# Performance work log

Measured on AMD Instinct MI355X. Metric: run time of the kernel, lower is better.

The kernel has to match this reference:

```python
import jax, jax.numpy as jnp
import numpy as np
from jax import lax

C = 512          # in_channels = n_feats of EDSR upsampler
HEADS = 8
NUM_SA = 8
NB = 8           # EDSR resblocks (assumed; source of make_edsr_baseline not provided)
NCLS = 6
SCALE = 2        # EDSR upsampling factor
IN_SCOPE = [(-51.2, 51.2, 3.2), (-51.2, 51.2, 3.2)]
OUT_SCOPE = [(-50.0, 50.0, 2.0), (-50.0, 50.0, 2.0)]


def setup_inputs() -> dict:
    key = jax.random.key(0)
    ks = jax.random.split(key, 16)
    n = lambda k, s: jax.random.normal(k, s, jnp.float32)
    s_lin = C ** -0.5
    s_c3 = (C * 9) ** -0.5
    d = {}
    d['x'] = n(ks[0], (1, C, 32, 32))
    # attention params (weights stored as (in, out) for direct matmul)
    d['qkv_w'] = n(ks[1], (NUM_SA, C, 3 * C)) * s_lin
    d['proj_w'] = n(ks[2], (NUM_SA, C, C)) * s_lin
    d['proj_b'] = jnp.zeros((NUM_SA, C), jnp.float32)
    # EDSR baseline params (OIHW conv kernels)
    d['head_w'] = n(ks[3], (C, C, 3, 3)) * s_c3
    d['head_b'] = jnp.zeros((C,), jnp.float32)
    d['body_w'] = n(ks[4], (NB, 2, C, C, 3, 3)) * s_c3
    d['body_b'] = jnp.zeros((NB, 2, C), jnp.float32)
    d['btail_w'] = n(ks[5], (C, C, 3, 3)) * s_c3
    d['btail_b'] = jnp.zeros((C,), jnp.float32)
    d['up_w'] = n(ks[6], (SCALE * SCALE * C, C, 3, 3)) * s_c3
    d['up_b'] = jnp.zeros((SCALE * SCALE * C,), jnp.float32)
    d['tail_w'] = n(ks[7], (C, C, 3, 3)) * s_c3
    d['tail_b'] = jnp.zeros((C,), jnp.float32)
    # classifier_hr: conv3(no bias)-BN-ReLU x2 + conv1
    d['c1_w'] = n(ks[8], (C, C, 3, 3)) * s_c3
    d['bn1_g'] = jnp.ones((C,), jnp.float32)
    d['bn1_b'] = jnp.zeros((C,), jnp.float32)
    d['bn1_m'] = jnp.zeros((C,), jnp.float32)
    d['bn1_v'] = jnp.ones((C,), jnp.float32)
    d['c2_w'] = n(ks[9], (C, C, 3, 3)) * s_c3
    d['bn2_g'] = jnp.ones((C,), jnp.float32)
    d['bn2_b'] = jnp.zeros((C,), jnp.float32)
    d['bn2_m'] = jnp.zeros((C,), jnp.float32)
    d['bn2_v'] = jnp.ones((C,), jnp.float32)
    d['c3_w'] = n(ks[10], (NCLS, C, 1, 1)) * s_lin
    d['c3_b'] = jnp.zeros((NCLS,), jnp.float32)
    return d


def _conv(x, w, b=None, pad=1):
    y = lax.conv_general_dilated(x, w, (1, 1), [(pad, pad), (pad, pad)],
                                 dimension_numbers=('NCHW', 'OIHW', 'NCHW'))
    return y if b is None else y + b[None, :, None, None]


def _bn(x, g, b, m, v):
    scale = (g / jnp.sqrt(v + 1e-5))[None, :, None, None]
    return (x - m[None, :, None, None]) * scale + b[None, :, None, None]


def _pixel_shuffle(x, r):
    B, Cr2, H, W = x.shape
    c = Cr2 // (r * r)
    return x.reshape(B, c, r, r, H, W).transpose(0, 1, 4, 2, 5, 3).reshape(B, c, H * r, W * r)


def _grid_idx(size, inscope, outscope):
    # nearest-neighbor grid_sample indices, align_corners=False, zeros padding
    imin, imax, _ = inscope
    omin, omax, ostep = outscope
    vv = jnp.arange(omin + ostep / 2, omax, ostep, dtype=jnp.float32)
    g = (vv - imin) / (imax - imin) * 2 - 1              # normalized coord in [-1,1]
    f = ((g + 1) * size - 1) / 2                          # unnormalize (align_corners=False)
    ii = jnp.round(f).astype(jnp.int32)
    valid = (ii >= 0) & (ii < size)
    return jnp.clip(ii, 0, size - 1), valid


def reference(x, qkv_w, proj_w, proj_b, head_w, head_b, body_w, body_b, btail_w, btail_b,
              up_w, up_b, tail_w, tail_b, c1_w, bn1_g, bn1_b, bn1_m, bn1_v,
              c2_w, bn2_g, bn2_b, bn2_m, bn2_v, c3_w, c3_b):
    B, Cc, H, W = x.shape
    hd = Cc // HEADS
    scale = Cc ** -0.5  # NOTE: source scales by in_channels**-0.5, not head_dim
    # --- num_sa manual self-attention blocks over H*W tokens ---
    for i in range(NUM_SA):
        t = x.reshape(B, Cc, H * W).transpose(0, 2, 1)            # (B, N, C)
        qkv = (t @ qkv_w[i]).reshape(B, H * W, 3, HEADS, hd).transpose(2, 0, 3, 1, 4)
        q, k, v = qkv[0], qkv[1], qkv[2]                          # (B, h, N, d)
        attn = jax.nn.softmax(jnp.einsum('bhnd,bhmd->bhnm', q, k) * scale, axis=-1)
        res = jnp.einsum('bhnm,bhmd->bhnd', attn, v).transpose(0, 2, 1, 3).reshape(B, H * W, Cc)
        res = (res @ proj_w[i] + proj_b[i]).reshape(B, H, W, Cc).transpose(0, 3, 1, 2)
        x = x + res
    # --- BEVGridTransform: nearest grid_sample ---
    iy, my = _grid_idx(H, IN_SCOPE[0], OUT_SCOPE[0])
    ix, mx = _grid_idx(W, IN_SCOPE[1], OUT_SCOPE[1])
    xs = x[:, :, iy[:, None], ix[None, :]] * (my[:, None] & mx[None, :]).astype(x.dtype)
    xs = lax.stop_gradient(xs)  # upsampler(x.detach())
    # --- EDSR baseline upsampler ---
    h = _conv(xs, head_w, head_b)
    r = h
    for i in range(NB):
        t = jax.nn.relu(_conv(r, body_w[i, 0], body_b[i, 0]))
        r = r + _conv(t, body_w[i, 1], body_b[i, 1])
    r = _conv(r, btail_w, btail_b) + h
    u = _pixel_shuffle(_conv(r, up_w, up_b), SCALE)
    y = _conv(u, tail_w, tail_b)
    # --- classifier_hr (BN in eval mode) ---
    y = jax.nn.relu(_bn(_conv(y, c1_w), bn1_g, bn1_b, bn1_m, bn1_v))
    y = jax.nn.relu(_bn(_conv(y, c2_w), bn2_g, bn2_b, bn2_m, bn2_v))
    y = _conv(y, c3_w, c3_b, pad=0)
    return jax.nn.sigmoid(y)  # eval path: (1, 6, 100, 100)
```

## Files before the change

kernel.cpp:

```cpp
#include <hip/hip_runtime.h>
#include <math.h>

#define DIV_UP(a,b) (((a)+(b)-1)/(b))

typedef __bf16 bf16x8 __attribute__((ext_vector_type(8)));
typedef float floatx4 __attribute__((ext_vector_type(4)));
typedef unsigned short u16;

__device__ __forceinline__ u16 f2bf(float f) {
    unsigned u = __builtin_bit_cast(unsigned, f);
    u = (u + 0x7fffu + ((u >> 16) & 1u)) >> 16;
    return (u16)u;
}
__device__ __forceinline__ float bf2f(u16 h) {
    unsigned u = ((unsigned)h) << 16;
    return __builtin_bit_cast(float, u);
}

__device__ __forceinline__ void gll16(const void* g, void* l) {
    __builtin_amdgcn_global_load_lds(
        (const __attribute__((address_space(1))) void*)g,
        (__attribute__((address_space(3))) void*)l, 16, 0, 0);
}

template<int BM, int BN, int GWM, int GWN>
__global__ __launch_bounds__(256) void gemm3_nt(
    const u16* __restrict__ Ah, const u16* __restrict__ Al,
    int lda, long long a_bs,
    const u16* __restrict__ Bh, const u16* __restrict__ Bl,
    int ldb, long long b_bs,
    float* C, u16* Ch, u16* Cl, int ldc, long long c_bs,
    const float* resid, int M, int N, int K, float alpha,
    const float* __restrict__ bias_m, const float* __restrict__ scale_m,
    const float* __restrict__ bias_n, int relu)
{
    constexpr int WTM = BM / GWM, WTN = BN / GWN;
    constexpr int TM = WTM / 16, TN = WTN / 16;
    __shared__ u16 Ash[BM * 32];
    __shared__ u16 Asl[BM * 32];
    __shared__ u16 Bsh[BN * 32];
    __shared__ u16 Bsl[BN * 32];
    const int tid = threadIdx.x;
    const int lane = tid & 63;
    const int w = tid >> 6;
    const int wm = (w % GWM) * WTM, wn = (w / GWM) * WTN;
    const int m0 = blockIdx.y * BM, n0 = blockIdx.x * BN;
    const int z = blockIdx.z;
    const u16* Ahb = Ah + (long long)z * a_bs;
    const u16* Alb = Al + (long long)z * a_bs;
    const u16* Bhb = Bh + (long long)z * b_bs;
    const u16* Blb = Bl + (long long)z * b_bs;
    const int quad = lane >> 4;

    floatx4 acc[TM][TN];
    #pragma unroll
    for (int i = 0; i < TM; ++i)
        #pragma unroll
        for (int j = 0; j < TN; ++j)
            #pragma unroll
            for (int r = 0; r < 4; ++r) acc[i][j][r] = 0.f;

    for (int kt = 0; kt < K; kt += 32) {
        #pragma unroll
        for (int p = 0; p < BM / 64; ++p) {
            int idx = p * 256 + tid;
            int row = idx >> 2;
            int olog = (idx & 3) ^ ((row >> 1) & 3);
            int gr = m0 + row; if (gr > M - 1) gr = M - 1;
            long long go = (long long)gr * lda + kt + olog * 8;
            gll16(Ahb + go, &Ash[idx * 8]);
            gll16(Alb + go, &Asl[idx * 8]);
        }
        #pragma unroll
        for (int p = 0; p < BN / 64; ++p) {
            int idx = p * 256 + tid;
            int row = idx >> 2;
            int olog = (idx & 3) ^ ((row >> 1) & 3);
            int gr = n0 + row; if (gr > N - 1) gr = N - 1;
            long long go = (long long)gr * ldb + kt + olog * 8;
            gll16(Bhb + go, &Bsh[idx * 8]);
            gll16(Blb + go, &Bsl[idx * 8]);
        }
        __syncthreads();

        bf16x8 afh[TM], afl[TM], bfh[TN], bfl[TN];
        #pragma unroll
        for (int i = 0; i < TM; ++i) {
            int row = wm + i * 16 + (lane & 15);
            int oph = quad ^ ((row >> 1) & 3);
            afh[i] = *(const bf16x8*)&Ash[row * 32 + oph * 8];
            afl[i] = *(const bf16x8*)&Asl[row * 32 + oph * 8];
        }
        #pragma unroll
        for (int j = 0; j < TN; ++j) {
            int row = wn + j * 16 + (lane & 15);
            int oph = quad ^ ((row >> 1) & 3);
            bfh[j] = *(const bf16x8*)&Bsh[row * 32 + oph * 8];
            bfl[j] = *(const bf16x8*)&Bsl[row * 32 + oph * 8];
        }
        #pragma unroll
        for (int i = 0; i < TM; ++i)
            #pragma unroll
            for (int j = 0; j < TN; ++j) {
                acc[i][j] = __builtin_amdgcn_mfma_f32_16x16x32_bf16(afh[i], bfl[j], acc[i][j], 0, 0, 0);
                acc[i][j] = __builtin_amdgcn_mfma_f32_16x16x32_bf16(afl[i], bfh[j], acc[i][j], 0, 0, 0);
                acc[i][j] = __builtin_amdgcn_mfma_f32_16x16x32_bf16(afh[i], bfh[j], acc[i][j], 0, 0, 0);
            }
        __syncthreads();
    }

    #pragma unroll
    for (int i = 0; i < TM; ++i) {
        int mbase = m0 + wm + i * 16 + quad * 4;
        #pragma unroll
        for (int j = 0; j < TN; ++j) {
            int n = n0 + wn + j * 16 + (lane & 15);
            if (n >= N) continue;
            float bn_ = bias_n ? bias_n[n] : 0.f;
            #pragma unroll
            for (int r = 0; r < 4; ++r) {
                int m = mbase + r;
                if (m >= M) continue;
                float t = acc[i][j][r] * alpha;
                if (scale_m) t *= scale_m[m];
                if (bias_m)  t += bias_m[m];
                t += bn_;
                long long idx = (long long)z * c_bs + (long long)m * ldc + n;
                if (resid) t += resid[idx];
                if (relu) t = fmaxf(t, 0.f);
                if (C)  C[idx] = t;
                if (Ch) {
                    u16 h = f2bf(t);
                    Ch[idx] = h;
                    Cl[idx] = f2bf(t - bf2f(h));
                }
            }
        }
    }
}

template<int BM, int BN, int GWM, int GWN>
__global__ __launch_bounds__(256) void conv_gemm(
    const u16* __restrict__ Ih, const u16* __restrict__ Il,
    const u16* __restrict__ Wh, const u16* __restrict__ Wl,
    int Wd, int pW, int M, int N, int kper,
    float* __restrict__ Cp,
    float* __restrict__ C, u16* __restrict__ Ph, u16* __restrict__ Pl,
    const float* __restrict__ resid, const float* __restrict__ bias_n,
    const float* __restrict__ scale_n, int relu)
{
    constexpr int WTM = BM / GWM, WTN = BN / GWN;
    constexpr int TM = WTM / 16, TN = WTN / 16;
    __shared__ u16 Ash[BM * 32];
    __shared__ u16 Asl[BM * 32];
    __shared__ u16 Bsh[BN * 32];
    __shared__ u16 Bsl[BN * 32];
    const int tid = threadIdx.x;
    const int lane = tid & 63;
    const int w = tid >> 6;
    const int wm = (w % GWM) * WTM, wn = (w / GWM) * WTN;
    const int m0 = blockIdx.y * BM, n0 = blockIdx.x * BN;
    const int quad = lane >> 4;

    long aoff[BM / 64];
    #pragma unroll
    for (int p = 0; p < BM / 64; ++p) {
        int idx = p * 256 + tid;
        int row = idx >> 2;
        int olog = (idx & 3) ^ ((row >> 1) & 3);
        int gr = m0 + row; if (gr > M - 1) gr = M - 1;
        int hh = gr / Wd, ww = gr - hh * Wd;
        aoff[p] = ((long)(hh + 1) * pW + (ww + 1)) * 512 + olog * 8;
    }
    long boff[BN / 64];
    #pragma unroll
    for (int p = 0; p < BN / 64; ++p) {
        int idx = p * 256 + tid;
        int row = idx >> 2;
        int olog = (idx & 3) ^ ((row >> 1) & 3);
        int gn = n0 + row; if (gn > N - 1) gn = N - 1;
        boff[p] = (long)gn * 4608 + olog * 8;
    }

    floatx4 acc[TM][TN];
    #pragma unroll
    for (int i = 0; i < TM; ++i)
        #pragma unroll
        for (int j = 0; j < TN; ++j)
            #pragma unroll
            for (int r = 0; r < 4; ++r) acc[i][j][r] = 0.f;

    const int k0 = blockIdx.z * kper, k1 = k0 + kper;
    for (int kt = k0; kt < k1; kt += 32) {
        int r = kt >> 9;
        int rd = r / 3;
        long roff = ((long)(rd - 1) * pW + (r - 3 * rd - 1)) * 512 + (kt & 511);
        #pragma unroll
        for (int p = 0; p < BM / 64; ++p) {
            long go = aoff[p] + roff;
            gll16(Ih + go, &Ash[(p * 256 + tid) * 8]);
            gll16(Il + go, &Asl[(p * 256 + tid) * 8]);
        }
        #pragma unroll
        for (int p = 0; p < BN / 64; ++p) {
            long go = boff[p] + kt;
            gll16(Wh + go, &Bsh[(p * 256 + tid) * 8]);
            gll16(Wl + go, &Bsl[(p * 256 + tid) * 8]);
        }
        __syncthreads();

        bf16x8 afh[TM], afl[TM], bfh[TN], bfl[TN];
        #pragma unroll
        for (int i = 0; i < TM; ++i) {
            int row = wm + i * 16 + (lane & 15);
            int oph = quad ^ ((row >> 1) & 3);
            afh[i] = *(const bf16x8*)&Ash[row * 32 + oph * 8];
            afl[i] = *(const bf16x8*)&Asl[row * 32 + oph * 8];
        }
        #pragma unroll
        for (int j = 0; j < TN; ++j) {
            int row = wn + j * 16 + (lane & 15);
            int oph = quad ^ ((row >> 1) & 3);
            bfh[j] = *(const bf16x8*)&Bsh[row * 32 + oph * 8];
            bfl[j] = *(const bf16x8*)&Bsl[row * 32 + oph * 8];
        }
        #pragma unroll
        for (int i = 0; i < TM; ++i)
            #pragma unroll
            for (int j = 0; j < TN; ++j) {
                acc[i][j] = __builtin_amdgcn_mfma_f32_16x16x32_bf16(afh[i], bfl[j], acc[i][j], 0, 0, 0);
                acc[i][j] = __builtin_amdgcn_mfma_f32_16x16x32_bf16(afl[i], bfh[j], acc[i][j], 0, 0, 0);
                acc[i][j] = __builtin_amdgcn_mfma_f32_16x16x32_bf16(afh[i], bfh[j], acc[i][j], 0, 0, 0);
            }
        __syncthreads();
    }

    const long zoff = (long)blockIdx.z * M * N;
    #pragma unroll
    for (int i = 0; i < TM; ++i) {
        int mbase = m0 + wm + i * 16 + quad * 4;
        #pragma unroll
        for (int j = 0; j < TN; ++j) {
            int n = n0 + wn + j * 16 + (lane & 15);
            if (n >= N) continue;
            float bn_ = bias_n ? bias_n[n] : 0.f;
            float sn_ = scale_n ? scale_n[n] : 1.f;
            #pragma unroll
            for (int rr = 0; rr < 4; ++rr) {
                int m = mbase + rr;
                if (m >= M) continue;
                long li = (long)m * N + n;
                if (Cp) { Cp[zoff + li] = acc[i][j][rr]; continue; }
                float t = acc[i][j][rr] * sn_ + bn_;
                if (resid) t += resid[li];
                if (relu) t = fmaxf(t, 0.f);
                if (C) C[li] = t;
                if (Ph) {
                    int hh = m / Wd, ww = m - hh * Wd;
                    long po = ((long)(hh + 1) * pW + ww + 1) * N + n;
                    u16 h2 = f2bf(t);
                    Ph[po] = h2;
                    Pl[po] = f2bf(t - bf2f(h2));
                }
            }
        }
    }
}

__global__ __launch_bounds__(256) void reduce_ep(
    const float* __restrict__ Cp, int KS, int M, int N, int Wd, int pW,
    float* __restrict__ C, u16* __restrict__ Ph, u16* __restrict__ Pl,
    const float* __restrict__ resid, const float* __restrict__ bias_n,
    const float* __restrict__ scale_n, int relu)
{
    long i4 = (long)blockIdx.x * 256 + threadIdx.x;
    long MN = (long)M * N;
    if (i4 * 4 >= MN) return;
    long n4t = MN >> 2;
    float4 s = ((const float4*)Cp)[i4];
    for (int z = 1; z < KS; ++z) {
        float4 v = ((const float4*)Cp)[(long)z * n4t + i4];
        s.x += v.x; s.y += v.y; s.z += v.z; s.w += v.w;
    }
    long bse = i4 * 4;
    int n0 = (int)(bse % N);
    int m = (int)(bse / N);
    float t[4] = {s.x, s.y, s.z, s.w};
    #pragma unroll
    for (int e = 0; e < 4; ++e) {
        int n = n0 + e;
        if (scale_n) t[e] *= scale_n[n];
        if (bias_n)  t[e] += bias_n[n];
        if (resid)   t[e] += resid[bse + e];
        if (relu)    t[e] = fmaxf(t[e], 0.f);
    }
    if (C) {
        float4 o; o.x = t[0]; o.y = t[1]; o.z = t[2]; o.w = t[3];
        ((float4*)C)[i4] = o;
    }
    if (Ph) {
        int hh = m / Wd, ww = m - hh * Wd;
        long po = ((long)(hh + 1) * pW + ww + 1) * N + n0;
        ushort4 vh, vl;
        vh.x = f2bf(t[0]); vl.x = f2bf(t[0] - bf2f(vh.x));
        vh.y = f2bf(t[1]); vl.y = f2bf(t[1] - bf2f(vh.y));
        vh.z = f2bf(t[2]); vl.z = f2bf(t[2] - bf2f(vh.z));
        vh.w = f2bf(t[3]); vl.w = f2bf(t[3] - bf2f(vh.w));
        *(ushort4*)(Ph + po) = vh;
        *(ushort4*)(Pl + po) = vl;
    }
}

__global__ __launch_bounds__(256) void wreorder(const float* __restrict__ w,
                                                u16* __restrict__ Wh,
                                                u16* __restrict__ Wl, int total)
{
    int i = blockIdx.x * 256 + threadIdx.x;
    if (i >= total) return;
    int co = i / 4608;
    int k = i - co * 4608;
    int r = k >> 9, ci = k & 511;
    float v = w[co * 4608 + ci * 9 + r];
    u16 h = f2bf(v);
    Wh[i] = h;
    Wl[i] = f2bf(v - bf2f(h));
}

__global__ __launch_bounds__(256) void zero_f4(float4* p, int n4)
{
    int i = blockIdx.x * 256 + threadIdx.x;
    if (i < n4) { float4 z; z.x = z.y = z.z = z.w = 0.f; p[i] = z; }
}

__global__ __launch_bounds__(256) void xpose_cast2(const float* __restrict__ src,
                                                   u16* __restrict__ dh,
                                                   u16* __restrict__ dl,
                                                   int R, int Cc)
{
    __shared__ float tile[32][33];
    const int z = blockIdx.z;
    const float* s = src + (long long)z * R * Cc;
    const long long zb = (long long)z * R * Cc;
    const int c0 = blockIdx.x * 32, r0 = blockIdx.y * 32;
    const int tc = threadIdx.x & 31, tr = threadIdx.x >> 5;
    #pragma unroll
    for (int q = 0; q < 4; ++q)
        tile[tr + q * 8][tc] = s[(long long)(r0 + tr + q * 8) * Cc + c0 + tc];
    __syncthreads();
    #pragma unroll
    for (int q = 0; q < 4; ++q) {
        float v = tile[tc][tr + q * 8];
        long long o = zb + (long long)(c0 + tr + q * 8) * R + r0 + tc;
        u16 h = f2bf(v);
        dh[o] = h;
        dl[o] = f2bf(v - bf2f(h));
    }
}

__global__ __launch_bounds__(256) void xpose_x2(const float* __restrict__ x,
                                                float* __restrict__ X32,
                                                u16* __restrict__ Xh,
                                                u16* __restrict__ Xl)
{
    __shared__ float tile[32][33];
    const int t0 = blockIdx.x * 32;
    const int c0 = blockIdx.y * 32;
    const int tc = threadIdx.x & 31, tr = threadIdx.x >> 5;
    #pragma unroll
    for (int q = 0; q < 4; ++q)
        tile[tr + q * 8][tc] = x[(long long)(c0 + tr + q * 8) * 1024 + t0 + tc];
    __syncthreads();
    #pragma unroll
    for (int q = 0; q < 4; ++q) {
        int tok = t0 + tr + q * 8, c = c0 + tc;
        float v = tile[tc][tr + q * 8];
        long long o = (long long)tok * 512 + c;
        X32[o] = v;
        u16 h = f2bf(v);
        Xh[o] = h;
        Xl[o] = f2bf(v - bf2f(h));
    }
}

__global__ __launch_bounds__(256) void vt_xpose2(const u16* __restrict__ Qh,
                                                 const u16* __restrict__ Ql,
                                                 u16* __restrict__ VTh,
                                                 u16* __restrict__ VTl)
{
    __shared__ u16 th[32][34];
    __shared__ u16 tl[32][34];
    const int c0 = blockIdx.x * 32;
    const int r0 = blockIdx.y * 32;
    const int tc = threadIdx.x & 31, tr = threadIdx.x >> 5;
    #pragma unroll
    for (int q = 0; q < 4; ++q) {
        long long o = (long long)(r0 + tr + q * 8) * 1536 + 1024 + c0 + tc;
        th[tr + q * 8][tc] = Qh[o];
        tl[tr + q * 8][tc] = Ql[o];
    }
    __syncthreads();
    #pragma unroll
    for (int q = 0; q < 4; ++q) {
        long long o = (long long)(c0 + tr + q * 8) * 1024 + r0 + tc;
        VTh[o] = th[tc][tr + q * 8];
        VTl[o] = tl[tc][tr + q * 8];
    }
}

__global__ __launch_bounds__(256) void softmax_bf2(const float* __restrict__ S,
                                                   u16* __restrict__ Ph,
                                                   u16* __restrict__ Pl)
{
    __shared__ float rmax[4], rsum[4];
    const long long base = (long long)blockIdx.x * 1024;
    const int t = threadIdx.x;
    float4 v = *(const float4*)(S + base + t * 4);
    float mx = fmaxf(fmaxf(v.x, v.y), fmaxf(v.z, v.w));
    #pragma unroll
    for (int o = 32; o > 0; o >>= 1) mx = fmaxf(mx, __shfl_down(mx, o));
    if ((t & 63) == 0) rmax[t >> 6] = mx;
    __syncthreads();
    float m4 = fmaxf(fmaxf(rmax[0], rmax[1]), fmaxf(rmax[2], rmax[3]));
    v.x = expf(v.x - m4); v.y = expf(v.y - m4);
    v.z = expf(v.z - m4); v.w = expf(v.w - m4);
    float sm = v.x + v.y + v.z + v.w;
    #pragma unroll
    for (int o = 32; o > 0; o >>= 1) sm += __shfl_down(sm, o);
    if ((t & 63) == 0) rsum[t >> 6] = sm;
    __syncthreads();
    float inv = 1.f / (rsum[0] + rsum[1] + rsum[2] + rsum[3]);
    float p0 = v.x * inv, p1 = v.y * inv, p2 = v.z * inv, p3 = v.w * inv;
    ushort4 oh, ol;
    oh.x = f2bf(p0); ol.x = f2bf(p0 - bf2f(oh.x));
    oh.y = f2bf(p1); ol.y = f2bf(p1 - bf2f(oh.y));
    oh.z = f2bf(p2); ol.z = f2bf(p2 - bf2f(oh.z));
    oh.w = f2bf(p3); ol.w = f2bf(p3 - bf2f(oh.w));
    *(ushort4*)(Ph + base + t * 4) = oh;
    *(ushort4*)(Pl + base + t * 4) = ol;
}

__global__ __launch_bounds__(256) void grid_sample_p(const float* __restrict__ X,
                                                     u16* __restrict__ Ph,
                                                     u16* __restrict__ Pl)
{
    int idx = blockIdx.x * 256 + threadIdx.x;
    if (idx >= 2500 * 512) return;
    int c = idx & 511;
    int p = idx >> 9;
    int i = p / 50, j = p - i * 50;
    float vy = -49.f + 2.f * i;
    float gy = (vy + 51.2f) / 102.4f * 2.f - 1.f;
    float fy = ((gy + 1.f) * 32.f - 1.f) * 0.5f;
    int iy = (int)roundf(fy);
    bool oky = (iy >= 0) && (iy < 32);
    iy = min(max(iy, 0), 31);
    float vx = -49.f + 2.f * j;
    float gx = (vx + 51.2f) / 102.4f * 2.f - 1.f;
    float fx = ((gx + 1.f) * 32.f - 1.f) * 0.5f;
    int ix = (int)roundf(fx);
    bool okx = (ix >= 0) && (ix < 32);
    ix = min(max(ix, 0), 31);
    int tok = iy * 32 + ix;
    float v = (oky && okx) ? X[(long)tok * 512 + c] : 0.f;
    long po = ((long)(i + 1) * 52 + (j + 1)) * 512 + c;
    u16 h = f2bf(v);
    Ph[po] = h;
    Pl[po] = f2bf(v - bf2f(h));
}

__global__ __launch_bounds__(256) void pixshuf_p(const float* __restrict__ up,
                                                 u16* __restrict__ Ph,
                                                 u16* __restrict__ Pl)
{
    int idx = blockIdx.x * 256 + threadIdx.x;
    if (idx >= 10000 * 512) return;
    int c = idx & 511;
    int p = idx >> 9;
    int oh = p / 100, ow = p - oh * 100;
    int h = oh >> 1, r1 = oh & 1, w2 = ow >> 1, r2 = ow & 1;
    float v = up[(long)(h * 50 + w2) * 2048 + (c << 2) + (r1 << 1) + r2];
    long po = ((long)(oh + 1) * 102 + (ow + 1)) * 512 + c;
    u16 hh = f2bf(v);
    Ph[po] = hh;
    Pl[po] = f2bf(v - bf2f(hh));
}

__global__ __launch_bounds__(256) void bnprep(
    const float* g1, const float* b1, const float* m1, const float* v1,
    const float* g2, const float* b2, const float* m2, const float* v2,
    float* sc1, float* bi1, float* sc2, float* bi2)
{
    int c = blockIdx.x * 256 + threadIdx.x;
    if (c >= 512) return;
    float s1 = g1[c] * rsqrtf(v1[c] + 1e-5f);
    sc1[c] = s1; bi1[c] = b1[c] - m1[c] * s1;
    float s2 = g2[c] * rsqrtf(v2[c] + 1e-5f);
    sc2[c] = s2; bi2[c] = b2[c] - m2[c] * s2;
}

__global__ __launch_bounds__(256) void conv1x1_sig_h(const float* __restrict__ in,
                                                     const float* __restrict__ w,
                                                     const float* __restrict__ b,
                                                     float* __restrict__ out)
{
    int pix = blockIdx.x * 4 + (threadIdx.x >> 6);
    int lane = threadIdx.x & 63;
    const float* row = in + (long)pix * 512;
    float4 a0 = *(const float4*)(row + lane * 8);
    float4 a1 = *(const float4*)(row + lane * 8 + 4);
    float s[6];
    #pragma unroll
    for (int co = 0; co < 6; ++co) {
        const float* wr = w + co * 512 + lane * 8;
        float4 w0 = *(const float4*)wr;
        float4 w1 = *(const float4*)(wr + 4);
        s[co] = a0.x * w0.x + a0.y * w0.y + a0.z * w0.z + a0.w * w0.w
              + a1.x * w1.x + a1.y * w1.y + a1.z * w1.z + a1.w * w1.w;
    }
    #pragma unroll
    for (int co = 0; co < 6; ++co)
        #pragma unroll
        for (int o = 32; o > 0; o >>= 1) s[co] += __shfl_xor(s[co], o);
    if (lane < 6) {
        float t = s[lane] + b[lane];
        out[lane * 10000 + pix] = 1.f / (1.f + expf(-t));
    }
}

extern "C" void kernel_launch(void* const* d_in, const int* in_sizes, int n_in,
                              void* d_out, int out_size, void* d_ws, size_t ws_size,
                              hipStream_t stream)
{
    const float* x      = (const float*)d_in[0];
    const float* qkv_w  = (const float*)d_in[1];
    const float* proj_w = (const float*)d_in[2];
    const float* proj_b = (const float*)d_in[3];
    const float* head_w = (const float*)d_in[4];
    const float* head_b = (const float*)d_in[5];
    const float* body_w = (const float*)d_in[6];
    const float* body_b = (const float*)d_in[7];
    const float* btail_w= (const float*)d_in[8];
    const float* btail_b= (const float*)d_in[9];
    const float* up_w   = (const float*)d_in[10];
    const float* up_b   = (const float*)d_in[11];
    const float* tail_w = (const float*)d_in[12];
    const float* tail_b = (const float*)d_in[13];
    const float* c1_w   = (const float*)d_in[14];
    const float* bn1_g  = (const float*)d_in[15];
    const float* bn1_b  = (const float*)d_in[16];
    const float* bn1_m  = (const float*)d_in[17];
    const float* bn1_v  = (const float*)d_in[18];
    const float* c2_w   = (const float*)d_in[19];
    const float* bn2_g  = (const float*)d_in[20];
    const float* bn2_b  = (const float*)d_in[21];
    const float* bn2_m  = (const float*)d_in[22];
    const float* bn2_v  = (const float*)d_in[23];
    const float* c3_w   = (const float*)d_in[24];
    const float* c3_b   = (const float*)d_in[25];

    char* base = (char*)d_ws;
    float*          S    = (float*)(base + 0);
    u16*            P_h  = (u16*)(base + 33554432);
    u16*            P_l  = (u16*)(base + 50331648);
    u16*            Q_h  = (u16*)(base + 67108864);
    u16*            Q_l  = (u16*)(base + 70254592);
    u16*            VT_h = (u16*)(base + 73400320);
    u16*            VT_l = (u16*)(base + 74448896);
    u16*            qw_h = (u16*)(base + 75497472);
    u16*            qw_l = (u16*)(base + 88080384);
    u16*            pw_h = (u16*)(base + 100663296);
    u16*            pw_l = (u16*)(base + 104857600);
    u16*            O_h  = (u16*)(base + 109051904);
    u16*            O_l  = (u16*)(base + 110100480);
    float*          X32b = (float*)(base + 111149056);
    u16*            X_h  = (u16*)(base + 113246208);
    u16*            X_l  = (u16*)(base + 114294784);
    float*          X32a = (float*)(base + 115343360);
    u16*   WB_h = (u16*)(base + 0);
    u16*   WB_l = (u16*)(base + 18874368);
    u16*   PX_h = (u16*)(base + 37748736);
    u16*   PX_l = (u16*)(base + 40517632);
    u16*   PA_h = (u16*)(base + 43286528);
    u16*   PA_l = (u16*)(base + 46055424);
    u16*   PB_h = (u16*)(base + 48824320);
    u16*   PB_l = (u16*)(base + 51593216);
    float* HhF  = (float*)(base + 54362112);
    float* RF1  = (float*)(base + 59482112);
    float* RF2  = (float*)(base + 64602112);
    float* Cp   = (float*)(base + 69722112);
    float* UPF  = (float*)(base + 85082112);
    float* Z2F  = (float*)(base + 85082112);
    u16*   PU_h = (u16*)(base + 105562112);
    u16*   PU_l = (u16*)(base + 116215808);
    u16*   PY_h = (u16*)(base + 126869504);
    u16*   PY_l = (u16*)(base + 137523200);
    float* SC1  = (float*)(base + 151494656);
    float* BI1  = SC1 + 512;
    float* SC2  = BI1 + 512;
    float* BI2  = SC2 + 512;

    const float scale = 0.044194173824159216f;

    xpose_cast2<<<dim3(48, 16, 8), 256, 0, stream>>>(qkv_w, qw_h, qw_l, 512, 1536);
    xpose_cast2<<<dim3(16, 16, 8), 256, 0, stream>>>(proj_w, pw_h, pw_l, 512, 512);
    xpose_x2<<<dim3(32, 16), 256, 0, stream>>>(x, X32a, X_h, X_l);

    for (int i = 0; i < 8; ++i) {
        float* Xold = (i % 2 == 0) ? X32a : X32b;
        float* Xnew = (i % 2 == 0) ? X32b : X32a;
        gemm3_nt<64, 128, 1, 4><<<dim3(12, 16, 1), 256, 0, stream>>>(
            X_h, X_l, 512, 0, qw_h + (long long)i * 786432, qw_l + (long long)i * 786432, 512, 0,
            nullptr, Q_h, Q_l, 1536, 0, nullptr, 1024, 1536, 512, 1.f,
            nullptr, nullptr, nullptr, 0);
        gemm3_nt<128, 128, 2, 2><<<dim3(8, 8, 8), 256, 0, stream>>>(
            Q_h, Q_l, 1536, 64, Q_h + 512, Q_l + 512, 1536, 64,
            S, nullptr, nullptr, 1024, 1048576, nullptr, 1024, 1024, 64, scale,
            nullptr, nullptr, nullptr, 0);
        softmax_bf2<<<8192, 256, 0, stream>>>(S, P_h, P_l);
        vt_xpose2<<<dim3(16, 32), 256, 0, stream>>>(Q_h, Q_l, VT_h, VT_l);
        gemm3_nt<64, 64, 1, 4><<<dim3(1, 16, 8), 256, 0, stream>>>(
            P_h, P_l, 1024, 1048576, VT_h, VT_l, 1024, 65536,
            nullptr, O_h, O_l, 512, 64, nullptr, 1024, 64, 1024, 1.f,
            nullptr, nullptr, nullptr, 0);
        gemm3_nt<64, 64, 1, 4><<<dim3(8, 16, 1), 256, 0, stream>>>(
            O_h, O_l, 512, 0, pw_h + (long long)i * 262144, pw_l + (long long)i * 262144, 512, 0,
            Xnew, X_h, X_l, 512, 0, Xold, 1024, 512, 512, 1.f,
            nullptr, nullptr, proj_b + i * 512, 0);
    }

    zero_f4<<<DIV_UP(1038336, 256), 256, 0, stream>>>((float4*)(base + 37748736), 1038336);
    grid_sample_p<<<DIV_UP(1280000, 256), 256, 0, stream>>>(X32a, PX_h, PX_l);
    zero_f4<<<DIV_UP(2663424, 256), 256, 0, stream>>>((float4*)(base + 105562112), 2663424);

    auto convK = [&](const u16* iPh, const u16* iPl, int H, int Wd,
                     const float* wsrc, int Cout, const float* bias, const float* scl,
                     const float* resid, int relu,
                     float* outC, u16* oPh, u16* oPl) {
        int pW = Wd + 2, M = H * Wd;
        int tot = Cout * 4608;
        wreorder<<<DIV_UP(tot, 256), 256, 0, stream>>>(wsrc, WB_h, WB_l, tot);
        if (Cout == 512 && M == 2500) {
            conv_gemm<128, 64, 2, 2><<<dim3(8, DIV_UP(M, 128), 3), 256, 0, stream>>>(
                iPh, iPl, WB_h, WB_l, Wd, pW, M, 512, 1536, Cp,
                nullptr, nullptr, nullptr, nullptr, nullptr, nullptr, 0);
            reduce_ep<<<DIV_UP(M * 512 / 4, 256), 256, 0, stream>>>(
                Cp, 3, M, 512, Wd, pW, outC, oPh, oPl, resid, bias, scl, relu);
        } else if (Cout == 2048) {
            conv_gemm<128, 128, 2, 2><<<dim3(16, DIV_UP(M, 128), 1), 256, 0, stream>>>(
                iPh, iPl, WB_h, WB_l, Wd, pW, M, 2048, 4608, nullptr,
                outC, oPh, oPl, resid, bias, scl, relu);
        } else {
            conv_gemm<128, 128, 2, 2><<<dim3(4, DIV_UP(M, 128), 1), 256, 0, stream>>>(
                iPh, iPl, WB_h, WB_l, Wd, pW, M, 512, 4608, nullptr,
                outC, oPh, oPl, resid, bias, scl, relu);
        }
    };

    convK(PX_h, PX_l, 50, 50, head_w, 512, head_b, nullptr, nullptr, 0, HhF, PA_h, PA_l);
    const float* rres = HhF;
    float* RFs[2] = {RF1, RF2};
    for (int i = 0; i < 8; ++i) {
        convK(PA_h, PA_l, 50, 50, body_w + (long long)(2 * i) * 2359296, 512,
              body_b + 2 * i * 512, nullptr, nullptr, 1, nullptr, PB_h, PB_l);
        float* Rout = RFs[i & 1];
        convK(PB_h, PB_l, 50, 50, body_w + (long long)(2 * i + 1) * 2359296, 512,
              body_b + (2 * i + 1) * 512, nullptr, rres, 0, Rout, PA_h, PA_l);
        rres = Rout;
    }
    convK(PA_h, PA_l, 50, 50, btail_w, 512, btail_b, nullptr, HhF, 0, nullptr, PB_h, PB_l);
    convK(PB_h, PB_l, 50, 50, up_w, 2048, up_b, nullptr, nullptr, 0, UPF, nullptr, nullptr);
    pixshuf_p<<<DIV_UP(5120000, 256), 256, 0, stream>>>(UPF, PU_h, PU_l);
    convK(PU_h, PU_l, 100, 100, tail_w, 512, tail_b, nullptr, nullptr, 0, nullptr, PY_h, PY_l);

    bnprep<<<2, 256, 0, stream>>>(bn1_g, bn1_b, bn1_m, bn1_v,
                                  bn2_g, bn2_b, bn2_m, bn2_v, SC1, BI1, SC2, BI2);
    convK(PY_h, PY_l, 100, 100, c1_w, 512, BI1, SC1, nullptr, 1, nullptr, PU_h, PU_l);
    convK(PU_h, PU_l, 100, 100, c2_w, 512, BI2, SC2, nullptr, 1, Z2F, nullptr, nullptr);
    conv1x1_sig_h<<<2500, 256, 0, stream>>>(Z2F, c3_w, c3_b, (float*)d_out);
}
```

Before: 3.353 ms.

## Double-buffer LDS tiles in GEMM and conv kernels to overlap loads with MFMA

Both the batched GEMM and implicit-GEMM conv kernels now keep two LDS buffers per operand. The next K-slice is prefetched with global_load_lds while the current slice is computed, and a partial vmcnt wait lets the prefetch stay in flight. This hides global-load latency that the single-buffer loop exposed at every step. It doubles LDS use per block, which may lower occupancy, and correctness depends on hand-written waitcnt and barrier ordering.

```diff
diff --git a/kernel.cpp b/kernel.cpp
--- a/kernel.cpp
+++ b/kernel.cpp
@@ -36,10 +36,11 @@
 {
     constexpr int WTM = BM / GWM, WTN = BN / GWN;
     constexpr int TM = WTM / 16, TN = WTN / 16;
-    __shared__ u16 Ash[BM * 32];
-    __shared__ u16 Asl[BM * 32];
-    __shared__ u16 Bsh[BN * 32];
-    __shared__ u16 Bsl[BN * 32];
+    constexpr int NLD = (BM / 64) * 2 + (BN / 64) * 2;
+    __shared__ u16 Ash[2][BM * 32];
+    __shared__ u16 Asl[2][BM * 32];
+    __shared__ u16 Bsh[2][BN * 32];
+    __shared__ u16 Bsl[2][BN * 32];
     const int tid = threadIdx.x;
     const int lane = tid & 63;
     const int w = tid >> 6;
@@ -60,7 +61,7 @@
             #pragma unroll
             for (int r = 0; r < 4; ++r) acc[i][j][r] = 0.f;
 
-    for (int kt = 0; kt < K; kt += 32) {
+    auto stage = [&](int kt, int buf) {
         #pragma unroll
         for (int p = 0; p < BM / 64; ++p) {
             int idx = p * 256 + tid;
@@ -68,8 +69,8 @@
             int olog = (idx & 3) ^ ((row >> 1) & 3);
             int gr = m0 + row; if (gr > M - 1) gr = M - 1;
             long long go = (long long)gr * lda + kt + olog * 8;
-            gll16(Ahb + go, &Ash[idx * 8]);
-            gll16(Alb + go, &Asl[idx * 8]);
+            gll16(Ahb + go, &Ash[buf][idx * 8]);
+            gll16(Alb + go, &Asl[buf][idx * 8]);
         }
         #pragma unroll
         for (int p = 0; p < BN / 64; ++p) {
@@ -78,25 +79,37 @@
             int olog = (idx & 3) ^ ((row >> 1) & 3);
             int gr = n0 + row; if (gr > N - 1) gr = N - 1;
             long long go = (long long)gr * ldb + kt + olog * 8;
-            gll16(Bhb + go, &Bsh[idx * 8]);
-            gll16(Blb + go, &Bsl[idx * 8]);
-        }
-        __syncthreads();
+            gll16(Bhb + go, &Bsh[buf][idx * 8]);
+            gll16(Blb + go, &Bsl[buf][idx * 8]);
+        }
+    };
+
+    stage(0, 0);
+    int cur = 0;
+    for (int kt = 0; kt < K; kt += 32) {
+        if (kt + 32 < K) {
+            stage(kt + 32, cur ^ 1);
+            asm volatile("s_waitcnt vmcnt(%0)" :: "n"(NLD) : "memory");
+        } else {
+            asm volatile("s_waitcnt vmcnt(0)" ::: "memory");
+        }
+        __builtin_amdgcn_s_barrier();
+        asm volatile("" ::: "memory");
 
         bf16x8 afh[TM], afl[TM], bfh[TN], bfl[TN];
         #pragma unroll
         for (int i = 0; i < TM; ++i) {
             int row = wm + i * 16 + (lane & 15);
             int oph = quad ^ ((row >> 1) & 3);
-            afh[i] = *(const bf16x8*)&Ash[row * 32 + oph * 8];
-            afl[i] = *(const bf16x8*)&Asl[row * 32 + oph * 8];
+            afh[i] = *(const bf16x8*)&Ash[cur][row * 32 + oph * 8];
+            afl[i] = *(const bf16x8*)&Asl[cur][row * 32 + oph * 8];
         }
         #pragma unroll
         for (int j = 0; j < TN; ++j) {
             int row = wn + j * 16 + (lane & 15);
             int oph = quad ^ ((row >> 1) & 3);
-            bfh[j] = *(const bf16x8*)&Bsh[row * 32 + oph * 8];
-            bfl[j] = *(const bf16x8*)&Bsl[row * 32 + oph * 8];
+            bfh[j] = *(const bf16x8*)&Bsh[cur][row * 32 + oph * 8];
+            bfl[j] = *(const bf16x8*)&Bsl[cur][row * 32 + oph * 8];
         }
         #pragma unroll
         for (int i = 0; i < TM; ++i)
@@ -106,7 +119,10 @@
                 acc[i][j] = __builtin_amdgcn_mfma_f32_16x16x32_bf16(afl[i], bfh[j], acc[i][j], 0, 0, 0);
                 acc[i][j] = __builtin_amdgcn_mfma_f32_16x16x32_bf16(afh[i], bfh[j], acc[i][j], 0, 0, 0);
             }
-        __syncthreads();
+
+        asm volatile("s_waitcnt lgkmcnt(0)" ::: "memory");
+        __builtin_amdgcn_s_barrier();
+        cur ^= 1;
     }
 
     #pragma unroll
@@ -151,10 +167,11 @@
 {
     constexpr int WTM = BM / GWM, WTN = BN / GWN;
     constexpr int TM = WTM / 16, TN = WTN / 16;
-    __shared__ u16 Ash[BM * 32];
-    __shared__ u16 Asl[BM * 32];
-    __shared__ u16 Bsh[BN * 32];
-    __shared__ u16 Bsl[BN * 32];
+    constexpr int NLD = (BM / 64) * 2 + (BN / 64) * 2;
+    __shared__ u16 Ash[2][BM * 32];
+    __shared__ u16 Asl[2][BM * 32];
+    __shared__ u16 Bsh[2][BN * 32];
+    __shared__ u16 Bsl[2][BN * 32];
     const int tid = threadIdx.x;
     const int lane = tid & 63;
     const int w = tid >> 6;
@@ -190,39 +207,51 @@
             #pragma unroll
             for (int r = 0; r < 4; ++r) acc[i][j][r] = 0.f;
 
-    const int k0 = blockIdx.z * kper, k1 = k0 + kper;
-    for (int kt = k0; kt < k1; kt += 32) {
+    auto stage = [&](int kt, int buf) {
         int r = kt >> 9;
         int rd = r / 3;
         long roff = ((long)(rd - 1) * pW + (r - 3 * rd - 1)) * 512 + (kt & 511);
         #pragma unroll
         for (int p = 0; p < BM / 64; ++p) {
             long go = aoff[p] + roff;
-            gll16(Ih + go, &Ash[(p * 256 + tid) * 8]);
-            gll16(Il + go, &Asl[(p * 256 + tid) * 8]);
+            gll16(Ih + go, &Ash[buf][(p * 256 + tid) * 8]);
+            gll16(Il + go, &Asl[buf][(p * 256 + tid) * 8]);
         }
         #pragma unroll
         for (int p = 0; p < BN / 64; ++p) {
             long go = boff[p] + kt;
-            gll16(Wh + go, &Bsh[(p * 256 + tid) * 8]);
-            gll16(Wl + go, &Bsl[(p * 256 + tid) * 8]);
-        }
-        __syncthreads();
+            gll16(Wh + go, &Bsh[buf][(p * 256 + tid) * 8]);
+            gll16(Wl + go, &Bsl[buf][(p * 256 + tid) * 8]);
+        }
+    };
+
+    const int k0 = blockIdx.z * kper, k1 = k0 + kper;
+    stage(k0, 0);
+    int cur = 0;
+    for (int kt = k0; kt < k1; kt += 32) {
+        if (kt + 32 < k1) {
+            stage(kt + 32, cur ^ 1);
+            asm volatile("s_waitcnt vmcnt(%0)" :: "n"(NLD) : "memory");
+        } else {
+            asm volatile("s_waitcnt vmcnt(0)" ::: "memory");
+        }
+        __builtin_amdgcn_s_barrier();
+        asm volatile("" ::: "memory");
 
         bf16x8 afh[TM], afl[TM], bfh[TN], bfl[TN];
         #pragma unroll
         for (int i = 0; i < TM; ++i) {
             int row = wm + i * 16 + (lane & 15);
             int oph = quad ^ ((row >> 1) & 3);
-            afh[i] = *(const bf16x8*)&Ash[row * 32 + oph * 8];
-            afl[i] = *(const bf16x8*)&Asl[row * 32 + oph * 8];
+            afh[i] = *(const bf16x8*)&Ash[cur][row * 32 + oph * 8];
+            afl[i] = *(const bf16x8*)&Asl[cur][row * 32 + oph * 8];
         }
         #pragma unroll
         for (int j = 0; j < TN; ++j) {
             int row = wn + j * 16 + (lane & 15);
             int oph = quad ^ ((row >> 1) & 3);
-            bfh[j] = *(const bf16x8*)&Bsh[row * 32 + oph * 8];
-            bfl[j] = *(const bf16x8*)&Bsl[row * 32 + oph * 8];
+            bfh[j] = *(const bf16x8*)&Bsh[cur][row * 32 + oph * 8];
+            bfl[j] = *(const bf16x8*)&Bsl[cur][row * 32 + oph * 8];
         }
         #pragma unroll
         for (int i = 0; i < TM; ++i)
@@ -232,7 +261,10 @@
                 acc[i][j] = __builtin_amdgcn_mfma_f32_16x16x32_bf16(afl[i], bfh[j], acc[i][j], 0, 0, 0);
                 acc[i][j] = __builtin_amdgcn_mfma_f32_16x16x32_bf16(afh[i], bfh[j], acc[i][j], 0, 0, 0);
             }
-        __syncthreads();
+
+        asm volatile("s_waitcnt lgkmcnt(0)" ::: "memory");
+        __builtin_amdgcn_s_barrier();
+        cur ^= 1;
     }
 
     const long zoff = (long)blockIdx.z * M * N;
```

After: 3.363 ms. About the same (+0.3%).
